# Kernel tuning notes

Measured on AMD Instinct MI355X. Metric: run time of the kernel, lower is better.

Reference implementation:

```python
import jax, jax.numpy as jnp
import numpy as np
import math

DIM = 2048
NUM_HEADS = 16
HEAD_DIM = DIM // NUM_HEADS
BATCH = 4
SEQ = 2048
ROPE_BASE = 10000.0


def setup_inputs() -> dict:
    key = jax.random.key(0)
    ks = jax.random.split(key, 6)
    s = 1.0 / math.sqrt(DIM)
    return {
        "x": jax.random.normal(ks[0], (BATCH, SEQ, DIM), dtype=jnp.float32),
        "Wq": jax.random.normal(ks[1], (DIM, DIM), dtype=jnp.float32) * s,
        "Wk": jax.random.normal(ks[2], (DIM, DIM), dtype=jnp.float32) * s,
        "Wv": jax.random.normal(ks[3], (DIM, DIM), dtype=jnp.float32) * s,
        "Wo": jax.random.normal(ks[4], (DIM, DIM), dtype=jnp.float32) * s,
        "bo": jnp.zeros((DIM,), dtype=jnp.float32),
    }


def _apply_rope(t, pos):
    # t: [B, H, S, D]; standard rotate-half RoPE per head
    d = t.shape[-1]
    inv_freq = 1.0 / (ROPE_BASE ** (jnp.arange(0, d, 2, dtype=jnp.float32) / d))  # [D/2]
    ang = pos.astype(jnp.float32)[:, None] * inv_freq[None, :]  # [S, D/2]
    cos = jnp.concatenate([jnp.cos(ang), jnp.cos(ang)], axis=-1)  # [S, D]
    sin = jnp.concatenate([jnp.sin(ang), jnp.sin(ang)], axis=-1)
    t1, t2 = t[..., : d // 2], t[..., d // 2:]
    rot = jnp.concatenate([-t2, t1], axis=-1)
    return t * cos + rot * sin


def reference(x, Wq, Wk, Wv, Wo, bo):
    B, S, D = x.shape
    H, Hd = NUM_HEADS, HEAD_DIM
    # projections (torch Linear: x @ W.T)
    q = (x @ Wq.T).reshape(B, S, H, Hd).transpose(0, 2, 1, 3)  # [B,H,S,Hd]
    k = (x @ Wk.T).reshape(B, S, H, Hd).transpose(0, 2, 1, 3)
    v = (x @ Wv.T).reshape(B, S, H, Hd).transpose(0, 2, 1, 3)
    pos = jnp.arange(S)
    q = _apply_rope(q, pos)
    k = _apply_rope(k, pos)
    scores = jnp.einsum("bhqd,bhkd->bhqk", q, k) / math.sqrt(Hd)
    causal = jnp.tril(jnp.ones((S, S), dtype=bool))
    scores = jnp.where(causal, scores, -1e9)
    w = jax.nn.softmax(scores, axis=-1)
    out = jnp.einsum("bhqk,bhkd->bhqd", w, v)  # [B,H,S,Hd]
    out = out.transpose(0, 2, 1, 3).reshape(B, S, D)
    return out @ Wo.T + bo
```

## Files before the change

### kernel.cpp

```cpp
#include <hip/hip_runtime.h>

#define BATCH 4
#define SEQ   2048
#define DIM   2048
#define NH    16
#define HD    128

typedef __bf16 bf16x8 __attribute__((ext_vector_type(8)));
typedef float  f32x4  __attribute__((ext_vector_type(4)));

__device__ __forceinline__ unsigned short f2bf(float f) {
  unsigned int u = __builtin_bit_cast(unsigned int, f);
  u += 0x7fffu + ((u >> 16) & 1u);
  return (unsigned short)(u >> 16);
}

__device__ __forceinline__ void async16(void* lds, const void* g) {
  __builtin_amdgcn_global_load_lds(
      (const __attribute__((address_space(1))) unsigned int*)g,
      (__attribute__((address_space(3))) unsigned int*)lds, 16, 0, 0);
}

__global__ __launch_bounds__(256) void cast_all_kernel(
    const float* __restrict__ x,
    const float* __restrict__ w0, const float* __restrict__ w1,
    const float* __restrict__ w2, const float* __restrict__ w3,
    unsigned short* __restrict__ dst) {
  int i = blockIdx.x * 256 + threadIdx.x;
  const float* s;
  int loc;
  if (i < (1 << 22)) { s = x; loc = i; }
  else {
    int k = i - (1 << 22);
    int sel = k >> 20; loc = k & 0xfffff;
    s = sel == 0 ? w0 : sel == 1 ? w1 : sel == 2 ? w2 : w3;
  }
  float4 v = ((const float4*)s)[loc];
  ushort4 o;
  o.x = f2bf(v.x); o.y = f2bf(v.y); o.z = f2bf(v.z); o.w = f2bf(v.w);
  ((ushort4*)dst)[i] = o;
}

__global__ __launch_bounds__(256) void gemm_qkv(
    const unsigned short* __restrict__ A,
    const unsigned short* __restrict__ Wq,
    const unsigned short* __restrict__ Wk,
    const unsigned short* __restrict__ Wv,
    unsigned short* __restrict__ Qo,
    unsigned short* __restrict__ Ko,
    unsigned short* __restrict__ Vto) {
  __shared__ unsigned short As[128 * 32];
  __shared__ unsigned short Bs[128 * 32];
  __shared__ float ep[32 * 132];
  const int tid = threadIdx.x;
  const int lane = tid & 63, wv = tid >> 6;
  const int q15 = lane & 15, quad = lane >> 4;
  const int wm = wv >> 1, wn = wv & 1;
  const int gx = blockIdx.x;
  const int sel = gx >> 4, h = gx & 15;
  const int m0 = blockIdx.y * 128;
  const unsigned short* Bw =
      (sel == 0 ? Wq : (sel == 1 ? Wk : Wv)) + (size_t)h * 128 * DIM;

  f32x4 acc[4][4] = {};

  for (int kt = 0; kt < DIM; kt += 32) {
    __syncthreads();
#pragma unroll
    for (int i = 0; i < 2; ++i) {
      int l = i * 256 + tid;
      int r = l >> 2, s = l & 3;
      int c = (s - (r >> 1)) & 3;
      async16(&As[l * 8], A + (size_t)(m0 + r) * DIM + kt + c * 8);
    }
#pragma unroll
    for (int i = 0; i < 2; ++i) {
      int l = i * 256 + tid;
      int r = l >> 2, s = l & 3;
      int c = (s - (r >> 1)) & 3;
      async16(&Bs[l * 8], Bw + (size_t)r * DIM + kt + c * 8);
    }
    __syncthreads();

    bf16x8 af[4], bf[4];
#pragma unroll
    for (int mf = 0; mf < 4; ++mf) {
      int r = wm * 64 + mf * 16 + q15;
      int sl = r * 4 + ((quad + (r >> 1)) & 3);
      af[mf] = *(const bf16x8*)&As[sl * 8];
    }
#pragma unroll
    for (int nf = 0; nf < 4; ++nf) {
      int r = wn * 64 + nf * 16 + q15;
      int sl = r * 4 + ((quad + (r >> 1)) & 3);
      bf[nf] = *(const bf16x8*)&Bs[sl * 8];
    }
#pragma unroll
    for (int mf = 0; mf < 4; ++mf)
#pragma unroll
      for (int nf = 0; nf < 4; ++nf)
        acc[mf][nf] = __builtin_amdgcn_mfma_f32_16x16x32_bf16(af[mf], bf[nf], acc[mf][nf], 0, 0, 0);
  }

  const int b = m0 >> 11;
  const int s0 = m0 & (SEQ - 1);
  const int bh = b * NH + h;
  const float CS = 0.12751744f;

  float invf[2][8];
  if (sel < 2) {
#pragma unroll
    for (int oi = 0; oi < 2; ++oi) {
      int oc = ((oi * 256 + tid) & 15) * 8;
#pragma unroll
      for (int j = 0; j < 8; ++j)
        invf[oi][j] = exp2f(-(float)((oc & 63) + j) * 0.20762050593046932f);
    }
  }

  for (int c = 0; c < 4; ++c) {
    __syncthreads();
    if (wm == (c >> 1)) {
      int mfb = (c & 1) * 2;
#pragma unroll
      for (int mi = 0; mi < 2; ++mi) {
        int mf = mfb + mi;
        int rr0 = mf * 16 + quad * 4 - (c & 1) * 32;
#pragma unroll
        for (int nf = 0; nf < 4; ++nf) {
          int col = wn * 64 + nf * 16 + q15;
#pragma unroll
          for (int r = 0; r < 4; ++r)
            ep[(rr0 + r) * 132 + col] = acc[mf][nf][r];
        }
      }
    }
    __syncthreads();
#pragma unroll
    for (int oi = 0; oi < 2; ++oi) {
      int o = oi * 256 + tid;
      if (sel < 2) {
        int rr = o >> 4, oc = (o & 15) * 8;
        int s = s0 + c * 32 + rr;
        float sf = (float)s;
        float4 a0 = *(const float4*)&ep[rr * 132 + oc];
        float4 a1 = *(const float4*)&ep[rr * 132 + oc + 4];
        float4 b0 = *(const float4*)&ep[rr * 132 + (oc ^ 64)];
        float4 b1 = *(const float4*)&ep[rr * 132 + (oc ^ 64) + 4];
        float av[8] = {a0.x, a0.y, a0.z, a0.w, a1.x, a1.y, a1.z, a1.w};
        float bv[8] = {b0.x, b0.y, b0.z, b0.w, b1.x, b1.y, b1.z, b1.w};
        float sgn = (oc & 64) ? 1.f : -1.f;
        float scl = (sel == 0) ? CS : 1.0f;
        unsigned short u[8];
#pragma unroll
        for (int j = 0; j < 8; ++j) {
          float ang = sf * invf[oi][j];
          float cc = __cosf(ang), ss = __sinf(ang);
          u[j] = f2bf((av[j] * cc + sgn * bv[j] * ss) * scl);
        }
        unsigned short* dst = (sel == 0 ? Qo : Ko) + ((size_t)bh * SEQ + s) * HD + oc;
        *(uint4*)dst = *(uint4*)u;
      } else {
        int hd = o & 127, so8 = (o >> 7) * 8;
        unsigned short u[8];
#pragma unroll
        for (int k = 0; k < 8; ++k)
          u[k] = f2bf(ep[(so8 + k) * 132 + hd]);
        *(uint4*)(Vto + ((size_t)bh * HD + hd) * SEQ + (s0 + c * 32 + so8)) = *(uint4*)u;
      }
    }
  }
}

__global__ __launch_bounds__(256) void gemm_out(
    const unsigned short* __restrict__ A,
    const unsigned short* __restrict__ Bw,
    float* __restrict__ outf,
    const float* __restrict__ bias) {
  __shared__ unsigned short As[128 * 32];
  __shared__ unsigned short Bs[128 * 32];
  const int tid = threadIdx.x;
  const int lane = tid & 63, wv = tid >> 6;
  const int q15 = lane & 15, quad = lane >> 4;
  const int wm = wv >> 1, wn = wv & 1;
  const int n0 = blockIdx.x * 128, m0 = blockIdx.y * 128;

  f32x4 acc[4][4] = {};

  for (int kt = 0; kt < DIM; kt += 32) {
    __syncthreads();
#pragma unroll
    for (int i = 0; i < 2; ++i) {
      int l = i * 256 + tid;
      int r = l >> 2, s = l & 3;
      int c = (s - (r >> 1)) & 3;
      async16(&As[l * 8], A + (size_t)(m0 + r) * DIM + kt + c * 8);
    }
#pragma unroll
    for (int i = 0; i < 2; ++i) {
      int l = i * 256 + tid;
      int r = l >> 2, s = l & 3;
      int c = (s - (r >> 1)) & 3;
      async16(&Bs[l * 8], Bw + (size_t)(n0 + r) * DIM + kt + c * 8);
    }
    __syncthreads();

    bf16x8 af[4], bf[4];
#pragma unroll
    for (int mf = 0; mf < 4; ++mf) {
      int r = wm * 64 + mf * 16 + q15;
      int sl = r * 4 + ((quad + (r >> 1)) & 3);
      af[mf] = *(const bf16x8*)&As[sl * 8];
    }
#pragma unroll
    for (int nf = 0; nf < 4; ++nf) {
      int r = wn * 64 + nf * 16 + q15;
      int sl = r * 4 + ((quad + (r >> 1)) & 3);
      bf[nf] = *(const bf16x8*)&Bs[sl * 8];
    }
#pragma unroll
    for (int mf = 0; mf < 4; ++mf)
#pragma unroll
      for (int nf = 0; nf < 4; ++nf)
        acc[mf][nf] = __builtin_amdgcn_mfma_f32_16x16x32_bf16(af[mf], bf[nf], acc[mf][nf], 0, 0, 0);
  }

#pragma unroll
  for (int mf = 0; mf < 4; ++mf)
#pragma unroll
    for (int nf = 0; nf < 4; ++nf) {
      int col = n0 + wn * 64 + nf * 16 + q15;
      float bv = bias[col];
#pragma unroll
      for (int r = 0; r < 4; ++r) {
        int row = m0 + wm * 64 + mf * 16 + quad * 4 + r;
        outf[(size_t)row * DIM + col] = acc[mf][nf][r] + bv;
      }
    }
}

__global__ __launch_bounds__(256) void attn_kernel(
    const unsigned short* __restrict__ Q,
    const unsigned short* __restrict__ Kg,
    const unsigned short* __restrict__ Vt,
    unsigned short* __restrict__ O) {
  __shared__ unsigned short Ks[64 * 128];
  __shared__ unsigned short Vs[128 * 64];
  __shared__ unsigned short Ps[4 * 32 * 72];
  const int tid = threadIdx.x;
  const int lane = tid & 63, wv = tid >> 6;
  const int q15 = lane & 15, quad = lane >> 4;
  const int bh = blockIdx.x & 63;
  const int t = blockIdx.x >> 6;
  const int nseg = (t < 8) ? 1 : 2;
  const int b = bh >> 4, h = bh & 15;
  unsigned short* Pw = Ps + wv * (32 * 72);

  for (int seg = 0; seg < nseg; ++seg) {
    const int qt = (t < 8) ? (15 - t) : (seg == 0 ? (15 - t) : (t - 8));
    const int q0w = qt * 128 + wv * 32;

    bf16x8 qf[2][4];
#pragma unroll
    for (int nq = 0; nq < 2; ++nq) {
      const unsigned short* qp = Q + ((size_t)bh * SEQ + q0w + nq * 16 + q15) * HD + quad * 8;
#pragma unroll
      for (int ks = 0; ks < 4; ++ks) qf[nq][ks] = *(const bf16x8*)(qp + ks * 32);
    }

    f32x4 oacc[2][8] = {};
    float rs[2] = {0.f, 0.f};
    const int jmax = 2 * qt + 2;
    const int jcap = 2 * qt + (wv >> 1);

    for (int j = 0; j < jmax; ++j) {
      const int kv0 = j * 64;
      __syncthreads();
#pragma unroll
      for (int i = 0; i < 4; ++i) {
        int l = i * 256 + tid;
        int r = l >> 4, c = (l & 15) ^ (r & 15);
        async16(&Ks[l * 8], Kg + ((size_t)bh * SEQ + kv0 + r) * HD + c * 8);
      }
#pragma unroll
      for (int i = 0; i < 4; ++i) {
        int l = i * 256 + tid;
        int r = l >> 3, c = (l & 7) ^ (r & 7);
        async16(&Vs[l * 8], Vt + ((size_t)bh * HD + r) * SEQ + kv0 + c * 8);
      }
      __syncthreads();

      if (j <= jcap) {
        const bool edge = (j == jcap);
#pragma unroll
        for (int mi = 0; mi < 4; ++mi) {
          f32x4 st[2] = {};
#pragma unroll
          for (int ks = 0; ks < 4; ++ks) {
            int r = mi * 16 + q15;
            int c = ks * 4 + quad;
            bf16x8 kf = *(const bf16x8*)&Ks[(r * 16 + (c ^ (r & 15))) * 8];
#pragma unroll
            for (int nq = 0; nq < 2; ++nq)
              st[nq] = __builtin_amdgcn_mfma_f32_16x16x32_bf16(kf, qf[nq][ks], st[nq], 0, 0, 0);
          }
#pragma unroll
          for (int nq = 0; nq < 2; ++nq) {
            unsigned int u[4];
#pragma unroll
            for (int r = 0; r < 4; ++r) {
              float p = exp2f(st[nq][r]);
              if (edge) {
                int kv = kv0 + mi * 16 + quad * 4 + r;
                int qq = q0w + nq * 16 + q15;
                p = (kv > qq) ? 0.f : p;
              }
              unsigned int uu = __builtin_bit_cast(unsigned int, p) & 0xffff0000u;
              rs[nq] += __builtin_bit_cast(float, uu);
              u[r] = uu;
            }
            uint2 pk;
            pk.x = (u[0] >> 16) | u[1];
            pk.y = (u[2] >> 16) | u[3];
            *(uint2*)&Pw[(nq * 16 + q15) * 72 + mi * 16 + quad * 4] = pk;
          }
        }
#pragma unroll
        for (int ks = 0; ks < 2; ++ks) {
          bf16x8 pf[2];
#pragma unroll
          for (int mq = 0; mq < 2; ++mq)
            pf[mq] = *(const bf16x8*)&Pw[(mq * 16 + q15) * 72 + ks * 32 + quad * 8];
#pragma unroll
          for (int nf = 0; nf < 8; ++nf) {
            int r = nf * 16 + q15;
            int c = ks * 4 + quad;
            bf16x8 vf = *(const bf16x8*)&Vs[(r * 8 + (c ^ (r & 7))) * 8];
#pragma unroll
            for (int mq = 0; mq < 2; ++mq)
              oacc[mq][nf] = __builtin_amdgcn_mfma_f32_16x16x32_bf16(pf[mq], vf, oacc[mq][nf], 0, 0, 0);
          }
        }
      }
    }

#pragma unroll
    for (int nq = 0; nq < 2; ++nq) {
      rs[nq] += __shfl_xor(rs[nq], 16);
      rs[nq] += __shfl_xor(rs[nq], 32);
    }
#pragma unroll
    for (int mq = 0; mq < 2; ++mq) {
#pragma unroll
      for (int r = 0; r < 4; ++r) {
        float l = __shfl(rs[mq], quad * 4 + r);
        float inv = 1.0f / l;
        int qq = q0w + mq * 16 + quad * 4 + r;
        size_t base = (((size_t)b * SEQ + qq) * NH + h) * HD;
#pragma unroll
        for (int nf = 0; nf < 8; ++nf)
          O[base + nf * 16 + q15] = f2bf(oacc[mq][nf][r] * inv);
      }
    }
  }
}

extern "C" void kernel_launch(void* const* d_in, const int* in_sizes, int n_in,
                              void* d_out, int out_size, void* d_ws, size_t ws_size,
                              hipStream_t stream) {
  (void)in_sizes; (void)n_in; (void)out_size; (void)ws_size;
  const float* x  = (const float*)d_in[0];
  const float* Wq = (const float*)d_in[1];
  const float* Wk = (const float*)d_in[2];
  const float* Wv = (const float*)d_in[3];
  const float* Wo = (const float*)d_in[4];
  const float* bo = (const float*)d_in[5];
  float* out = (float*)d_out;

  const size_t XE = (size_t)BATCH * SEQ * DIM;
  const size_t WE = (size_t)DIM * DIM;

  char* p = (char*)d_ws;
  unsigned short* xb   = (unsigned short*)p; p += XE * 2;
  unsigned short* Wall = (unsigned short*)p; p += 4 * WE * 2;
  unsigned short* Qg   = (unsigned short*)p; p += XE * 2;
  unsigned short* Kb   = (unsigned short*)p; p += XE * 2;
  unsigned short* Vtb  = (unsigned short*)p; p += XE * 2;
  unsigned short* attn = (unsigned short*)p; p += XE * 2;

  cast_all_kernel<<<(int)(2 * XE / 4 / 256), 256, 0, stream>>>(x, Wq, Wk, Wv, Wo, xb);

  gemm_qkv<<<dim3(48, 64), 256, 0, stream>>>(
      xb, Wall, Wall + WE, Wall + 2 * WE, Qg, Kb, Vtb);

  attn_kernel<<<dim3(768), 256, 0, stream>>>(Qg, Kb, Vtb, attn);

  gemm_out<<<dim3(DIM / 128, (BATCH * SEQ) / 128), 256, 0, stream>>>(
      attn, Wall + 3 * WE, out, bo);
}
```

Baseline: 687.8 us.

## Rewrite output GEMM as 256x256 double-buffered pipeline and prefetch K/V in attention

Replaces the output projection GEMM with a 512-thread kernel that computes a 256x256 tile. It uses 64-wide k-steps, double-buffered dynamic LDS (128KB), and interleaves async loads for the next tiles between quadrant MFMA batches, using barriers and setprio. The attention kernel now prefetches the next K/V tile into registers while computing on the current LDS tile, then commits it after a barrier. The aim is to hide global-load latency behind compute. The cost is much more LDS per block (fewer resident blocks), higher register pressure, and a fragile hand-tuned waitcnt schedule.

```diff
diff --git a/kernel.cpp b/kernel.cpp
--- a/kernel.cpp
+++ b/kernel.cpp
@@ -172,74 +172,112 @@
   }
 }
 
-__global__ __launch_bounds__(256) void gemm_out(
+#define STAGE8(buf, op, half, kt)                                               \
+  do {                                                                          \
+    const unsigned short* Gp = (op) ? Bw : A;                                   \
+    const int rb = ((op) ? n0 : m0) + (half) * 128;                             \
+    unsigned short* hb = sm + ((((buf) << 1) | (op)) * 2 + (half)) * 8192;      \
+    _Pragma("unroll")                                                           \
+    for (int jj = 0; jj < 2; ++jj) {                                            \
+      int l = jj * 512 + tid;                                                   \
+      int rr = l >> 3, cc = l & 7;                                              \
+      int cs = cc ^ (((rr >> 2) & 1) << 1);                                     \
+      async16(&hb[l * 8], Gp + (size_t)(rb + rr) * DIM + (kt) * 64 + cs * 8);   \
+    }                                                                           \
+  } while (0)
+
+#define RDA8(dst, buf, mf, ks)                                                  \
+  do {                                                                          \
+    int R = (mf) * 16 + q15;                                                    \
+    int cc = ((ks) * 4 + quad) ^ (((R >> 2) & 1) << 1);                         \
+    dst = *(const bf16x8*)&sm[((((buf) << 1) | 0) * 2 + wm) * 8192 + (R * 8 + cc) * 8]; \
+  } while (0)
+
+#define RDB8(dst, buf, nf, ks)                                                  \
+  do {                                                                          \
+    int R = (wn & 1) * 64 + (nf) * 16 + q15;                                    \
+    int cc = ((ks) * 4 + quad) ^ (((R >> 2) & 1) << 1);                         \
+    dst = *(const bf16x8*)&sm[((((buf) << 1) | 1) * 2 + (wn >> 1)) * 8192 + (R * 8 + cc) * 8]; \
+  } while (0)
+
+#define MFMA_Q(mlo, nlo)                                                        \
+  do {                                                                          \
+    __builtin_amdgcn_s_barrier();                                               \
+    asm volatile("s_waitcnt lgkmcnt(0)" ::: "memory");                          \
+    __builtin_amdgcn_sched_barrier(0);                                          \
+    __builtin_amdgcn_s_setprio(1);                                              \
+    _Pragma("unroll")                                                           \
+    for (int ks = 0; ks < 2; ++ks)                                              \
+      _Pragma("unroll")                                                         \
+      for (int mi = 0; mi < 4; ++mi)                                            \
+        _Pragma("unroll")                                                       \
+        for (int ni = 0; ni < 2; ++ni)                                          \
+          acc[(mlo) + mi][(nlo) + ni] = __builtin_amdgcn_mfma_f32_16x16x32_bf16( \
+              af[(mlo) + mi][ks], bfr[(nlo) + ni][ks], acc[(mlo) + mi][(nlo) + ni], 0, 0, 0); \
+    __builtin_amdgcn_s_setprio(0);                                              \
+    __builtin_amdgcn_sched_barrier(0);                                          \
+    __builtin_amdgcn_s_barrier();                                               \
+  } while (0)
+
+__global__ __launch_bounds__(512, 2) void gemm_out(
     const unsigned short* __restrict__ A,
     const unsigned short* __restrict__ Bw,
     float* __restrict__ outf,
     const float* __restrict__ bias) {
-  __shared__ unsigned short As[128 * 32];
-  __shared__ unsigned short Bs[128 * 32];
+  extern __shared__ unsigned short sm[];
   const int tid = threadIdx.x;
-  const int lane = tid & 63, wv = tid >> 6;
+  const int lane = tid & 63;
+  const int wv = tid >> 6;
   const int q15 = lane & 15, quad = lane >> 4;
-  const int wm = wv >> 1, wn = wv & 1;
-  const int n0 = blockIdx.x * 128, m0 = blockIdx.y * 128;
-
-  f32x4 acc[4][4] = {};
-
-  for (int kt = 0; kt < DIM; kt += 32) {
-    __syncthreads();
-#pragma unroll
-    for (int i = 0; i < 2; ++i) {
-      int l = i * 256 + tid;
-      int r = l >> 2, s = l & 3;
-      int c = (s - (r >> 1)) & 3;
-      async16(&As[l * 8], A + (size_t)(m0 + r) * DIM + kt + c * 8);
-    }
-#pragma unroll
-    for (int i = 0; i < 2; ++i) {
-      int l = i * 256 + tid;
-      int r = l >> 2, s = l & 3;
-      int c = (s - (r >> 1)) & 3;
-      async16(&Bs[l * 8], Bw + (size_t)(n0 + r) * DIM + kt + c * 8);
-    }
-    __syncthreads();
-
-    bf16x8 af[4], bf[4];
-#pragma unroll
-    for (int mf = 0; mf < 4; ++mf) {
-      int r = wm * 64 + mf * 16 + q15;
-      int sl = r * 4 + ((quad + (r >> 1)) & 3);
-      af[mf] = *(const bf16x8*)&As[sl * 8];
-    }
-#pragma unroll
-    for (int nf = 0; nf < 4; ++nf) {
-      int r = wn * 64 + nf * 16 + q15;
-      int sl = r * 4 + ((quad + (r >> 1)) & 3);
-      bf[nf] = *(const bf16x8*)&Bs[sl * 8];
-    }
-#pragma unroll
-    for (int mf = 0; mf < 4; ++mf)
-#pragma unroll
-      for (int nf = 0; nf < 4; ++nf)
-        acc[mf][nf] = __builtin_amdgcn_mfma_f32_16x16x32_bf16(af[mf], bf[nf], acc[mf][nf], 0, 0, 0);
-  }
-
-#pragma unroll
-  for (int mf = 0; mf < 4; ++mf)
+  const int wm = wv >> 2, wn = wv & 3;
+  const int n0 = blockIdx.x * 256, m0 = blockIdx.y * 256;
+
+  f32x4 acc[8][4] = {};
+  bf16x8 af[8][2], bfr[4][2];
+
+  STAGE8(0, 0, 0, 0); STAGE8(0, 0, 1, 0); STAGE8(0, 1, 0, 0); STAGE8(0, 1, 1, 0);
+  STAGE8(1, 0, 0, 1); STAGE8(1, 0, 1, 1);
+  asm volatile("s_waitcnt vmcnt(4)" ::: "memory");
+  __builtin_amdgcn_s_barrier();
+
+  for (int T = 0; T < 32; ++T) {
+    const int buf = T & 1;
+#pragma unroll
+    for (int mf = 0; mf < 4; ++mf) { RDA8(af[mf][0], buf, mf, 0); RDA8(af[mf][1], buf, mf, 1); }
+#pragma unroll
+    for (int nf = 0; nf < 2; ++nf) { RDB8(bfr[nf][0], buf, nf, 0); RDB8(bfr[nf][1], buf, nf, 1); }
+    if (T + 1 < 32) STAGE8(buf ^ 1, 1, 0, T + 1);
+    MFMA_Q(0, 0);
+#pragma unroll
+    for (int mf = 4; mf < 8; ++mf) { RDA8(af[mf][0], buf, mf, 0); RDA8(af[mf][1], buf, mf, 1); }
+#pragma unroll
+    for (int nf = 2; nf < 4; ++nf) { RDB8(bfr[nf][0], buf, nf, 0); RDB8(bfr[nf][1], buf, nf, 1); }
+    if (T + 1 < 32) STAGE8(buf ^ 1, 1, 1, T + 1);
+    MFMA_Q(0, 2);
+    if (T + 2 < 32) STAGE8(buf, 0, 0, T + 2);
+    MFMA_Q(4, 2);
+    if (T + 2 < 32) STAGE8(buf, 0, 1, T + 2);
+    if (T < 30) { asm volatile("s_waitcnt vmcnt(4)" ::: "memory"); }
+    else if (T == 30) { asm volatile("s_waitcnt vmcnt(0)" ::: "memory"); }
+    MFMA_Q(4, 0);
+  }
+
+  float bv[4];
+#pragma unroll
+  for (int nf = 0; nf < 4; ++nf) bv[nf] = bias[n0 + wn * 64 + nf * 16 + q15];
+#pragma unroll
+  for (int mf = 0; mf < 8; ++mf)
 #pragma unroll
     for (int nf = 0; nf < 4; ++nf) {
       int col = n0 + wn * 64 + nf * 16 + q15;
-      float bv = bias[col];
-#pragma unroll
-      for (int r = 0; r < 4; ++r) {
-        int row = m0 + wm * 64 + mf * 16 + quad * 4 + r;
-        outf[(size_t)row * DIM + col] = acc[mf][nf][r] + bv;
-      }
-    }
-}
-
-__global__ __launch_bounds__(256) void attn_kernel(
+      int row = m0 + wm * 128 + mf * 16 + quad * 4;
+#pragma unroll
+      for (int r = 0; r < 4; ++r)
+        outf[(size_t)(row + r) * DIM + col] = acc[mf][nf][r] + bv[nf];
+    }
+}
+
+__global__ __launch_bounds__(256, 3) void attn_kernel(
     const unsigned short* __restrict__ Q,
     const unsigned short* __restrict__ Kg,
     const unsigned short* __restrict__ Vt,
@@ -273,28 +311,44 @@
     const int jmax = 2 * qt + 2;
     const int jcap = 2 * qt + (wv >> 1);
 
-    for (int j = 0; j < jmax; ++j) {
-      const int kv0 = j * 64;
-      __syncthreads();
+    uint4 kreg[4], vreg[4];
+    auto issue = [&](int kv) {
 #pragma unroll
       for (int i = 0; i < 4; ++i) {
         int l = i * 256 + tid;
         int r = l >> 4, c = (l & 15) ^ (r & 15);
-        async16(&Ks[l * 8], Kg + ((size_t)bh * SEQ + kv0 + r) * HD + c * 8);
+        kreg[i] = *(const uint4*)(Kg + ((size_t)bh * SEQ + kv + r) * HD + c * 8);
       }
 #pragma unroll
       for (int i = 0; i < 4; ++i) {
         int l = i * 256 + tid;
         int r = l >> 3, c = (l & 7) ^ (r & 7);
-        async16(&Vs[l * 8], Vt + ((size_t)bh * HD + r) * SEQ + kv0 + c * 8);
-      }
-      __syncthreads();
+        vreg[i] = *(const uint4*)(Vt + ((size_t)bh * HD + r) * SEQ + kv + c * 8);
+      }
+    };
+    auto commit = [&]() {
+#pragma unroll
+      for (int i = 0; i < 4; ++i) { int l = i * 256 + tid; *(uint4*)&Ks[l * 8] = kreg[i]; }
+#pragma unroll
+      for (int i = 0; i < 4; ++i) { int l = i * 256 + tid; *(uint4*)&Vs[l * 8] = vreg[i]; }
+    };
+
+    issue(0);
+    commit();
+
+    for (int j = 0; j < jmax; ++j) {
+      const int kv0 = j * 64;
+      if (j + 1 < jmax) issue((j + 1) * 64);
+      asm volatile("s_waitcnt lgkmcnt(0)" ::: "memory");
+      __builtin_amdgcn_s_barrier();
+      __builtin_amdgcn_sched_barrier(0);
 
       if (j <= jcap) {
         const bool edge = (j == jcap);
 #pragma unroll
         for (int mi = 0; mi < 4; ++mi) {
           f32x4 st[2] = {};
+          __builtin_amdgcn_s_setprio(1);
 #pragma unroll
           for (int ks = 0; ks < 4; ++ks) {
             int r = mi * 16 + q15;
@@ -304,6 +358,7 @@
             for (int nq = 0; nq < 2; ++nq)
               st[nq] = __builtin_amdgcn_mfma_f32_16x16x32_bf16(kf, qf[nq][ks], st[nq], 0, 0, 0);
           }
+          __builtin_amdgcn_s_setprio(0);
 #pragma unroll
           for (int nq = 0; nq < 2; ++nq) {
             unsigned int u[4];
@@ -331,6 +386,7 @@
 #pragma unroll
           for (int mq = 0; mq < 2; ++mq)
             pf[mq] = *(const bf16x8*)&Pw[(mq * 16 + q15) * 72 + ks * 32 + quad * 8];
+          __builtin_amdgcn_s_setprio(1);
 #pragma unroll
           for (int nf = 0; nf < 8; ++nf) {
             int r = nf * 16 + q15;
@@ -340,8 +396,14 @@
             for (int mq = 0; mq < 2; ++mq)
               oacc[mq][nf] = __builtin_amdgcn_mfma_f32_16x16x32_bf16(pf[mq], vf, oacc[mq][nf], 0, 0, 0);
           }
+          __builtin_amdgcn_s_setprio(0);
         }
       }
+
+      asm volatile("s_waitcnt lgkmcnt(0)" ::: "memory");
+      __builtin_amdgcn_s_barrier();
+      __builtin_amdgcn_sched_barrier(0);
+      if (j + 1 < jmax) commit();
     }
 
 #pragma unroll
@@ -388,6 +450,13 @@
   unsigned short* Vtb  = (unsigned short*)p; p += XE * 2;
   unsigned short* attn = (unsigned short*)p; p += XE * 2;
 
+  static bool attr_set = false;
+  if (!attr_set) {
+    hipFuncSetAttribute((const void*)gemm_out,
+                        hipFuncAttributeMaxDynamicSharedMemorySize, 131072);
+    attr_set = true;
+  }
+
   cast_all_kernel<<<(int)(2 * XE / 4 / 256), 256, 0, stream>>>(x, Wq, Wk, Wv, Wo, xb);
 
   gemm_qkv<<<dim3(48, 64), 256, 0, stream>>>(
@@ -395,6 +464,6 @@
 
   attn_kernel<<<dim3(768), 256, 0, stream>>>(Qg, Kb, Vtb, attn);
 
-  gemm_out<<<dim3(DIM / 128, (BATCH * SEQ) / 128), 256, 0, stream>>>(
+  gemm_out<<<dim3(DIM / 256, (BATCH * SEQ) / 256), 512, 131072, stream>>>(
       attn, Wall + 3 * WE, out, bo);
 }
```

Measured after the change: 863.7 us. 25.6% more time.
